# Optimization experiments

Measured on AMD Instinct MI355X. Metric: run time of the kernel, lower is better.

## Reference

```python
import jax, jax.numpy as jnp
import numpy as np

B, T, CIN, H, W = 8, 16, 16, 64, 64
HID, K = 64, 3


def _conv(x, w, b):
    # x: [B, C, H, W], w: [O, C, K, K] -> [B, O, H, W], 'same' padding
    y = jax.lax.conv_general_dilated(x, w, window_strides=(1, 1), padding='SAME',
                                     dimension_numbers=('NCHW', 'OIHW', 'NCHW'))
    return y + b[None, :, None, None]


def setup_inputs() -> dict:
    key = jax.random.key(0)
    ks = jax.random.split(key, 9)
    cin_h = CIN + HID
    s_conv = 1.0 / np.sqrt(cin_h * K * K)
    s_lin = 1.0 / np.sqrt(cin_h)
    return {
        'x': jax.random.normal(ks[0], (B, T, CIN, H, W), dtype=jnp.float32),
        'Wf': jax.random.uniform(ks[1], (HID, cin_h, K, K), jnp.float32, -s_conv, s_conv),
        'bf': jax.random.uniform(ks[2], (HID,), jnp.float32, -s_conv, s_conv),
        'Wi': jax.random.uniform(ks[3], (HID, cin_h, K, K), jnp.float32, -s_conv, s_conv),
        'bi': jax.random.uniform(ks[4], (HID,), jnp.float32, -s_conv, s_conv),
        'Wc': jax.random.uniform(ks[5], (HID, cin_h, K, K), jnp.float32, -s_conv, s_conv),
        'bc': jax.random.uniform(ks[6], (HID,), jnp.float32, -s_conv, s_conv),
        'Wo': jax.random.uniform(ks[7], (HID, cin_h), jnp.float32, -s_lin, s_lin),
        'bo': jax.random.uniform(ks[8], (HID,), jnp.float32, -s_lin, s_lin),
    }


def reference(x, Wf, bf, Wi, bi, Wc, bc, Wo, bo):
    # x: [B, T, CIN, H, W]
    b, t, cin, h, w = x.shape
    h0 = jnp.zeros((b, HID, h, w), x.dtype)
    c0 = jnp.zeros((b, HID, h, w), x.dtype)

    def step(carry, xt):
        hs, cs = carry
        xc = jnp.concatenate([xt, hs], axis=1)          # [B, CIN+HID, H, W]
        f = jax.nn.sigmoid(_conv(xc, Wf, bf))
        i = jax.nn.sigmoid(_conv(xc, Wi, bi))
        g = jnp.tanh(_conv(xc, Wc, bc))
        # Linear over channel dim (torch applies it on transpose(1,3))
        o = jax.nn.sigmoid(jnp.einsum('bchw,oc->bohw', xc, Wo) + bo[None, :, None, None])
        cs = cs * f + i * g
        hs = jnp.tanh(cs) * o
        return (hs, cs), None

    xs = jnp.swapaxes(x, 0, 1)                          # time-major [T, B, CIN, H, W]
    (hT, cT), _ = jax.lax.scan(step, (h0, c0), xs)
    return hT, cT
```

## Files before the change

### kernel.cpp

```cpp
#include <hip/hip_runtime.h>


#define B_ 8
#define T_ 16
#define CIN_ 16
#define HID_ 64
#define H_ 64
#define W_ 64
#define HW_ (H_*W_)
#define CTOT_ 80
#define XS_ROW 34
#define XS_CH 104
#define XS_SIZE (3*XS_ROW*XS_CH)
#define CSTRIDE_ (B_*HID_*HW_)

typedef __attribute__((ext_vector_type(8))) short short8;
typedef __attribute__((ext_vector_type(4))) float f32x4;

__device__ __forceinline__ unsigned short f2bf(float f){
    unsigned u = __float_as_uint(f);
    u = (u + 0x7FFFu + ((u >> 16) & 1u)) >> 16;
    return (unsigned short)u;
}
__device__ __forceinline__ float sigm_(float v){ return 1.0f/(1.0f + __expf(-v)); }
__device__ __forceinline__ float tanh_(float v){ return 2.0f/(1.0f + __expf(-2.0f*v)) - 1.0f; }

__global__ void prep_wfrag(const float* __restrict__ Wf, const float* __restrict__ Wi,
                           const float* __restrict__ Wc, const float* __restrict__ Wo,
                           const float* __restrict__ bf, const float* __restrict__ bi,
                           const float* __restrict__ bc, const float* __restrict__ bo,
                           unsigned short* __restrict__ Wfrag){
    int idx = blockIdx.x*256 + threadIdx.x;
    int j    = idx & 7;
    int lane = (idx >> 3) & 63;
    int frag = idx >> 9;
    int ng = frag & 15;
    int tc = frag >> 4;
    int cc = tc % 3, tap = tc / 3;
    int n = ng*16 + (lane & 15);
    int g = n >> 6, o = n & 63;
    int c = cc*32 + ((lane >> 4) << 3) + j;
    int ky = tap / 3, kx = tap % 3;
    float v = 0.0f;
    if (c < CTOT_){
        if (g == 0)      v = Wf[((o*CTOT_ + c)*3 + ky)*3 + kx];
        else if (g == 1) v = Wi[((o*CTOT_ + c)*3 + ky)*3 + kx];
        else if (g == 2) v = Wc[((o*CTOT_ + c)*3 + ky)*3 + kx];
        else             v = (tap == 4) ? Wo[o*CTOT_ + c] : 0.0f;
    } else if (c == CTOT_ && tap == 4){
        v = (g==0) ? bf[o] : (g==1) ? bi[o] : (g==2) ? bc[o] : bo[o];
    }
    Wfrag[idx] = f2bf(v);
}

__global__ void prep_xbf(const float* __restrict__ x, unsigned short* __restrict__ xbf){
    int idx = blockIdx.x*256 + threadIdx.x;
    int px = idx & 63;
    int y  = (idx >> 6) & 63;
    int bt = idx >> 12;
    const float* src = x + (size_t)bt*CIN_*HW_ + y*W_ + px;
    unsigned short tmp[16];
    #pragma unroll
    for (int c = 0; c < 16; ++c) tmp[c] = f2bf(src[(size_t)c*HW_]);
    uint4* dst = (uint4*)(xbf + (size_t)idx*16);
    dst[0] = *(uint4*)(tmp);
    dst[1] = *(uint4*)(tmp + 8);
}

__global__ __launch_bounds__(256, 4) void lstm_step(
    const unsigned short* __restrict__ xbf,
    const unsigned short* __restrict__ Wfrag,
    float* __restrict__ cbuf,
    const unsigned short* __restrict__ hin,
    unsigned short* __restrict__ hout,
    float* __restrict__ out,
    int t)
{
    __shared__ __align__(16) unsigned short Xs[XS_SIZE];
    const int id   = blockIdx.x;
    const int xcd  = id & 7;
    const int jj   = id >> 3;
    const int y    = xcd*8 + (jj & 7);
    const int b    = (jj >> 3) & 7;
    const int half = jj >> 6;
    const int x0   = half*32;
    const int tid  = threadIdx.x;
    const int lane = tid & 63;
    const int w    = tid >> 6;
    const int l15  = lane & 15;
    const int q    = lane >> 4;

    uint4 z4; z4.x=z4.y=z4.z=z4.w=0u;
    for (int i = tid; i < XS_SIZE/8; i += 256) ((uint4*)Xs)[i] = z4;
    __syncthreads();

    for (int i = tid; i < 204; i += 256){
        int row = i/68, rem = i - row*68;
        int px = rem >> 1, ch8 = rem & 1;
        int yy = y + row - 1, pxg = x0 + px - 1;
        if (yy >= 0 && yy < H_ && pxg >= 0 && pxg < W_){
            uint4 v = *(const uint4*)(xbf + ((((size_t)(b*T_ + t)*H_ + yy)*W_ + pxg)*16 + ch8*8));
            *(uint4*)(Xs + (row*XS_ROW + px)*XS_CH + ch8*8) = v;
        }
    }
    if (t > 0){
        for (int i = tid; i < 816; i += 256){
            int row = i/272, rem = i - row*272;
            int px = rem >> 3, ch8 = rem & 7;
            int yy = y + row - 1, pxg = x0 + px - 1;
            if (yy >= 0 && yy < H_ && pxg >= 0 && pxg < W_){
                uint4 v = *(const uint4*)(hin + ((((size_t)b*H_ + yy)*W_ + pxg)*HID_ + ch8*8));
                *(uint4*)(Xs + (row*XS_ROW + px)*XS_CH + CIN_ + ch8*8) = v;
            }
        }
    }
    for (int i = tid; i < 3*XS_ROW; i += 256)
        Xs[i*XS_CH + CTOT_] = 0x3F80;
    __syncthreads();

    f32x4 acc[4][2];
    #pragma unroll
    for (int g = 0; g < 4; ++g){ acc[g][0] = (f32x4)0.0f; acc[g][1] = (f32x4)0.0f; }

    short8 aC[2], bC[3], bO;
    {
        const unsigned short* ap = Xs + (size_t)l15*XS_CH + q*8;
        aC[0] = *(const short8*)(ap);
        aC[1] = *(const short8*)(ap + 16*XS_CH);
        const unsigned short* bp = Wfrag + (size_t)w*512 + lane*8;
        #pragma unroll
        for (int g = 0; g < 3; ++g) bC[g] = *(const short8*)(bp + ((size_t)g << 11));
    }
    for (int cc = 0; cc < 3; ++cc){
        #pragma unroll 1
        for (int tap = 0; tap < 9; ++tap){
            int ncc = cc, ntap = tap + 1;
            if (ntap == 9){ ntap = 0; ++ncc; }
            const bool have = (ncc < 3);
            short8 aN[2], bN[3];
            if (have){
                const int nky = ntap/3, nkx = ntap - 3*(ntap/3);
                const unsigned short* ap =
                    Xs + (size_t)(nky*XS_ROW + l15 + nkx)*XS_CH + ncc*32 + q*8;
                aN[0] = *(const short8*)(ap);
                aN[1] = *(const short8*)(ap + 16*XS_CH);
                const unsigned short* bp =
                    Wfrag + ((size_t)((ntap*3 + ncc)*16 + w) << 9) + lane*8;
                #pragma unroll
                for (int g = 0; g < 3; ++g) bN[g] = *(const short8*)(bp + ((size_t)g << 11));
            }
            if (tap == 3)
                bO = *(const short8*)(Wfrag + ((size_t)((4*3 + cc)*16 + 12 + w) << 9) + lane*8);
            if (tap == 4){
                acc[3][0] = __builtin_amdgcn_mfma_f32_16x16x32_bf16(aC[0], bO, acc[3][0], 0,0,0);
                acc[3][1] = __builtin_amdgcn_mfma_f32_16x16x32_bf16(aC[1], bO, acc[3][1], 0,0,0);
            }
            #pragma unroll
            for (int g = 0; g < 3; ++g){
                acc[g][0] = __builtin_amdgcn_mfma_f32_16x16x32_bf16(aC[0], bC[g], acc[g][0], 0,0,0);
                acc[g][1] = __builtin_amdgcn_mfma_f32_16x16x32_bf16(aC[1], bC[g], acc[g][1], 0,0,0);
            }
            if (have){
                aC[0]=aN[0]; aC[1]=aN[1];
                bC[0]=bN[0]; bC[1]=bN[1]; bC[2]=bN[2];
            }
        }
    }

    const int o = w*16 + l15;
    #pragma unroll
    for (int mf = 0; mf < 2; ++mf){
        #pragma unroll
        for (int r = 0; r < 4; ++r){
            const int m = mf*16 + q*4 + r;
            const int pxg = x0 + m;
            const float fv = sigm_(acc[0][mf][r]);
            const float iv = sigm_(acc[1][mf][r]);
            const float gv = tanh_(acc[2][mf][r]);
            const float ov = sigm_(acc[3][mf][r]);
            const size_t cidx = (((size_t)(b*H_ + y)*W_ + pxg)*HID_ + o);
            const float cprev = t ? cbuf[cidx] : 0.0f;
            const float cn = cprev*fv + iv*gv;
            const float hn = tanh_(cn)*ov;
            if (t < T_-1){
                cbuf[cidx] = cn;
                hout[cidx] = f2bf(hn);
            } else {
                const size_t oidx = ((((size_t)(b*HID_ + o))*H_ + y)*W_ + pxg);
                out[oidx] = hn;
                out[CSTRIDE_ + oidx] = cn;
            }
        }
    }
}

extern "C" void kernel_launch(void* const* d_in, const int* in_sizes, int n_in,
                              void* d_out, int out_size, void* d_ws, size_t ws_size,
                              hipStream_t stream){
    const float* x  = (const float*)d_in[0];
    const float* Wf = (const float*)d_in[1];
    const float* bf = (const float*)d_in[2];
    const float* Wi = (const float*)d_in[3];
    const float* bi = (const float*)d_in[4];
    const float* Wc = (const float*)d_in[5];
    const float* bc = (const float*)d_in[6];
    const float* Wo = (const float*)d_in[7];
    const float* bo = (const float*)d_in[8];

    unsigned short* Wfrag = (unsigned short*)d_ws;
    unsigned short* xbf   = (unsigned short*)((char*)d_ws + 442368);
    float*          cbuf  = (float*)((char*)d_ws + 442368 + 16777216);
    unsigned short* hbfA  = (unsigned short*)((char*)d_ws + 442368 + 16777216 + 8388608);
    unsigned short* hbfB  = hbfA + CSTRIDE_;

    prep_wfrag<<<dim3(864), dim3(256), 0, stream>>>(Wf, Wi, Wc, Wo, bf, bi, bc, bo, Wfrag);
    prep_xbf<<<dim3(2048), dim3(256), 0, stream>>>(x, xbf);

    for (int t = 0; t < T_; ++t){
        const unsigned short* hi = (t & 1) ? hbfA : hbfB;
        unsigned short*       ho = (t & 1) ? hbfB : hbfA;
        lstm_step<<<dim3(1024), dim3(256), 0, stream>>>(
            xbf, Wfrag, cbuf, hi, ho, (float*)d_out, t);
    }
}
```

Baseline: 428.7 us.

## Process full image rows per block with deeper weight prefetch pipeline

Each block now computes a full 64-pixel row instead of half a row, doubling M-fragments per wave to reuse each loaded weight fragment across four MFMA rows and reducing halo reloads. The K-loop is fully unrolled with a three-slot ring buffer prefetching weights two steps ahead. This halves the grid to 512 blocks and raises LDS and register use, lowering occupancy and possibly leaving CUs underfilled.

```diff
diff --git a/kernel.cpp b/kernel.cpp
--- a/kernel.cpp
+++ b/kernel.cpp
@@ -9,7 +9,7 @@
 #define W_ 64
 #define HW_ (H_*W_)
 #define CTOT_ 80
-#define XS_ROW 34
+#define XS_ROW 66
 #define XS_CH 104
 #define XS_SIZE (3*XS_ROW*XS_CH)
 #define CSTRIDE_ (B_*HID_*HW_)
@@ -67,7 +67,7 @@
     dst[1] = *(uint4*)(tmp + 8);
 }
 
-__global__ __launch_bounds__(256, 4) void lstm_step(
+__global__ __launch_bounds__(256, 3) void lstm_step(
     const unsigned short* __restrict__ xbf,
     const unsigned short* __restrict__ Wfrag,
     float* __restrict__ cbuf,
@@ -82,8 +82,6 @@
     const int jj   = id >> 3;
     const int y    = xcd*8 + (jj & 7);
     const int b    = (jj >> 3) & 7;
-    const int half = jj >> 6;
-    const int x0   = half*32;
     const int tid  = threadIdx.x;
     const int lane = tid & 63;
     const int w    = tid >> 6;
@@ -94,20 +92,20 @@
     for (int i = tid; i < XS_SIZE/8; i += 256) ((uint4*)Xs)[i] = z4;
     __syncthreads();
 
-    for (int i = tid; i < 204; i += 256){
-        int row = i/68, rem = i - row*68;
+    for (int i = tid; i < 396; i += 256){
+        int row = i/132, rem = i - row*132;
         int px = rem >> 1, ch8 = rem & 1;
-        int yy = y + row - 1, pxg = x0 + px - 1;
+        int yy = y + row - 1, pxg = px - 1;
         if (yy >= 0 && yy < H_ && pxg >= 0 && pxg < W_){
             uint4 v = *(const uint4*)(xbf + ((((size_t)(b*T_ + t)*H_ + yy)*W_ + pxg)*16 + ch8*8));
             *(uint4*)(Xs + (row*XS_ROW + px)*XS_CH + ch8*8) = v;
         }
     }
     if (t > 0){
-        for (int i = tid; i < 816; i += 256){
-            int row = i/272, rem = i - row*272;
+        for (int i = tid; i < 1584; i += 256){
+            int row = i/528, rem = i - row*528;
             int px = rem >> 3, ch8 = rem & 7;
-            int yy = y + row - 1, pxg = x0 + px - 1;
+            int yy = y + row - 1, pxg = px - 1;
             if (yy >= 0 && yy < H_ && pxg >= 0 && pxg < W_){
                 uint4 v = *(const uint4*)(hin + ((((size_t)b*H_ + yy)*W_ + pxg)*HID_ + ch8*8));
                 *(uint4*)(Xs + (row*XS_ROW + px)*XS_CH + CIN_ + ch8*8) = v;
@@ -118,67 +116,71 @@
         Xs[i*XS_CH + CTOT_] = 0x3F80;
     __syncthreads();
 
-    f32x4 acc[4][2];
-    #pragma unroll
-    for (int g = 0; g < 4; ++g){ acc[g][0] = (f32x4)0.0f; acc[g][1] = (f32x4)0.0f; }
-
-    short8 aC[2], bC[3], bO;
+    f32x4 acc[4][4];
+    #pragma unroll
+    for (int g = 0; g < 4; ++g)
+        #pragma unroll
+        for (int mf = 0; mf < 4; ++mf) acc[g][mf] = (f32x4)0.0f;
+
+    short8 aC[4], bq[3][3], bqo[2];
     {
         const unsigned short* ap = Xs + (size_t)l15*XS_CH + q*8;
-        aC[0] = *(const short8*)(ap);
-        aC[1] = *(const short8*)(ap + 16*XS_CH);
-        const unsigned short* bp = Wfrag + (size_t)w*512 + lane*8;
-        #pragma unroll
-        for (int g = 0; g < 3; ++g) bC[g] = *(const short8*)(bp + ((size_t)g << 11));
-    }
-    for (int cc = 0; cc < 3; ++cc){
-        #pragma unroll 1
-        for (int tap = 0; tap < 9; ++tap){
-            int ncc = cc, ntap = tap + 1;
-            if (ntap == 9){ ntap = 0; ++ncc; }
-            const bool have = (ncc < 3);
-            short8 aN[2], bN[3];
-            if (have){
-                const int nky = ntap/3, nkx = ntap - 3*(ntap/3);
-                const unsigned short* ap =
-                    Xs + (size_t)(nky*XS_ROW + l15 + nkx)*XS_CH + ncc*32 + q*8;
-                aN[0] = *(const short8*)(ap);
-                aN[1] = *(const short8*)(ap + 16*XS_CH);
-                const unsigned short* bp =
-                    Wfrag + ((size_t)((ntap*3 + ncc)*16 + w) << 9) + lane*8;
-                #pragma unroll
-                for (int g = 0; g < 3; ++g) bN[g] = *(const short8*)(bp + ((size_t)g << 11));
-            }
-            if (tap == 3)
-                bO = *(const short8*)(Wfrag + ((size_t)((4*3 + cc)*16 + 12 + w) << 9) + lane*8);
-            if (tap == 4){
-                acc[3][0] = __builtin_amdgcn_mfma_f32_16x16x32_bf16(aC[0], bO, acc[3][0], 0,0,0);
-                acc[3][1] = __builtin_amdgcn_mfma_f32_16x16x32_bf16(aC[1], bO, acc[3][1], 0,0,0);
-            }
-            #pragma unroll
-            for (int g = 0; g < 3; ++g){
-                acc[g][0] = __builtin_amdgcn_mfma_f32_16x16x32_bf16(aC[0], bC[g], acc[g][0], 0,0,0);
-                acc[g][1] = __builtin_amdgcn_mfma_f32_16x16x32_bf16(aC[1], bC[g], acc[g][1], 0,0,0);
-            }
-            if (have){
-                aC[0]=aN[0]; aC[1]=aN[1];
-                bC[0]=bN[0]; bC[1]=bN[1]; bC[2]=bN[2];
-            }
+        #pragma unroll
+        for (int mf = 0; mf < 4; ++mf) aC[mf] = *(const short8*)(ap + (size_t)mf*16*XS_CH);
+        #pragma unroll
+        for (int kt = 0; kt < 2; ++kt){
+            const unsigned short* bp = Wfrag + ((size_t)(kt*3*16 + w) << 9) + lane*8;
+            #pragma unroll
+            for (int g = 0; g < 3; ++g) bq[kt][g] = *(const short8*)(bp + ((size_t)g << 11));
+        }
+    }
+    #pragma unroll
+    for (int kt = 0; kt < 27; ++kt){
+        const int tap = kt % 9, cc = kt / 9;
+        if (kt + 2 < 27){
+            const int pk = kt + 2, pt = pk % 9, pc = pk / 9;
+            const unsigned short* bp = Wfrag + ((size_t)((pt*3 + pc)*16 + w) << 9) + lane*8;
+            #pragma unroll
+            for (int g = 0; g < 3; ++g) bq[pk % 3][g] = *(const short8*)(bp + ((size_t)g << 11));
+            if (pt == 4)
+                bqo[pc & 1] = *(const short8*)(Wfrag + ((size_t)((4*3 + pc)*16 + 12 + w) << 9) + lane*8);
+        }
+        short8 aN[4];
+        if (kt + 1 < 27){
+            const int nk = kt + 1, nt = nk % 9, nc = nk / 9;
+            const int nky = nt / 3, nkx = nt % 3;
+            const unsigned short* ap =
+                Xs + (size_t)(nky*XS_ROW + l15 + nkx)*XS_CH + nc*32 + q*8;
+            #pragma unroll
+            for (int mf = 0; mf < 4; ++mf) aN[mf] = *(const short8*)(ap + (size_t)mf*16*XS_CH);
+        }
+        if (tap == 4){
+            #pragma unroll
+            for (int mf = 0; mf < 4; ++mf)
+                acc[3][mf] = __builtin_amdgcn_mfma_f32_16x16x32_bf16(aC[mf], bqo[cc & 1], acc[3][mf], 0,0,0);
+        }
+        #pragma unroll
+        for (int g = 0; g < 3; ++g)
+            #pragma unroll
+            for (int mf = 0; mf < 4; ++mf)
+                acc[g][mf] = __builtin_amdgcn_mfma_f32_16x16x32_bf16(aC[mf], bq[kt % 3][g], acc[g][mf], 0,0,0);
+        if (kt + 1 < 27){
+            #pragma unroll
+            for (int mf = 0; mf < 4; ++mf) aC[mf] = aN[mf];
         }
     }
 
     const int o = w*16 + l15;
     #pragma unroll
-    for (int mf = 0; mf < 2; ++mf){
+    for (int mf = 0; mf < 4; ++mf){
         #pragma unroll
         for (int r = 0; r < 4; ++r){
             const int m = mf*16 + q*4 + r;
-            const int pxg = x0 + m;
             const float fv = sigm_(acc[0][mf][r]);
             const float iv = sigm_(acc[1][mf][r]);
             const float gv = tanh_(acc[2][mf][r]);
             const float ov = sigm_(acc[3][mf][r]);
-            const size_t cidx = (((size_t)(b*H_ + y)*W_ + pxg)*HID_ + o);
+            const size_t cidx = (((size_t)(b*H_ + y)*W_ + m)*HID_ + o);
             const float cprev = t ? cbuf[cidx] : 0.0f;
             const float cn = cprev*fv + iv*gv;
             const float hn = tanh_(cn)*ov;
@@ -186,7 +188,7 @@
                 cbuf[cidx] = cn;
                 hout[cidx] = f2bf(hn);
             } else {
-                const size_t oidx = ((((size_t)(b*HID_ + o))*H_ + y)*W_ + pxg);
+                const size_t oidx = ((((size_t)(b*HID_ + o))*H_ + y)*W_ + m);
                 out[oidx] = hn;
                 out[CSTRIDE_ + oidx] = cn;
             }
@@ -219,7 +221,7 @@
     for (int t = 0; t < T_; ++t){
         const unsigned short* hi = (t & 1) ? hbfA : hbfB;
         unsigned short*       ho = (t & 1) ? hbfB : hbfA;
-        lstm_step<<<dim3(1024), dim3(256), 0, stream>>>(
+        lstm_step<<<dim3(512), dim3(256), 0, stream>>>(
             xbf, Wfrag, cbuf, hi, ho, (float*)d_out, t);
     }
 }
```

After: 474.8 us. 1.11x slower.

## Split K reduction across two wave groups per block with LDS partial-sum merge

Applied to the files above, without the earlier changes.

Doubles the block to 512 threads and splits the 27 (channel-chunk, tap) reduction steps between two groups of four waves. The second group writes its partial accumulators to shared memory and the first group adds them before the gate epilogue. At t=0 only the 9 input-channel steps are computed because h is zero, which skips work the old loop did on zero data. This raises the number of waves in flight per block to hide latency, at the cost of an extra barrier, an LDS round trip and an uneven split (13 vs 14 steps).

```diff
diff --git a/kernel.cpp b/kernel.cpp
--- a/kernel.cpp
+++ b/kernel.cpp
@@ -12,6 +12,8 @@
 #define XS_ROW 34
 #define XS_CH 104
 #define XS_SIZE (3*XS_ROW*XS_CH)
+#define SM_BYTES 32768
+#define KSPLIT 13
 #define CSTRIDE_ (B_*HID_*HW_)
 
 typedef __attribute__((ext_vector_type(8))) short short8;
@@ -67,7 +69,7 @@
     dst[1] = *(uint4*)(tmp + 8);
 }
 
-__global__ __launch_bounds__(256, 4) void lstm_step(
+__global__ __launch_bounds__(512, 4) void lstm_step(
     const unsigned short* __restrict__ xbf,
     const unsigned short* __restrict__ Wfrag,
     float* __restrict__ cbuf,
@@ -76,25 +78,29 @@
     float* __restrict__ out,
     int t)
 {
-    __shared__ __align__(16) unsigned short Xs[XS_SIZE];
+    __shared__ __align__(16) char smem[SM_BYTES];
+    unsigned short* Xs = (unsigned short*)smem;
+    float*          P  = (float*)smem;
+
     const int id   = blockIdx.x;
     const int xcd  = id & 7;
     const int jj   = id >> 3;
     const int y    = xcd*8 + (jj & 7);
     const int b    = (jj >> 3) & 7;
-    const int half = jj >> 6;
-    const int x0   = half*32;
+    const int x0   = (jj >> 6) * 32;
     const int tid  = threadIdx.x;
     const int lane = tid & 63;
     const int w    = tid >> 6;
+    const int wl   = w & 3;
+    const int wh   = w >> 2;
     const int l15  = lane & 15;
     const int q    = lane >> 4;
 
     uint4 z4; z4.x=z4.y=z4.z=z4.w=0u;
-    for (int i = tid; i < XS_SIZE/8; i += 256) ((uint4*)Xs)[i] = z4;
-    __syncthreads();
-
-    for (int i = tid; i < 204; i += 256){
+    for (int i = tid; i < XS_SIZE/8; i += 512) ((uint4*)Xs)[i] = z4;
+    __syncthreads();
+
+    for (int i = tid; i < 204; i += 512){
         int row = i/68, rem = i - row*68;
         int px = rem >> 1, ch8 = rem & 1;
         int yy = y + row - 1, pxg = x0 + px - 1;
@@ -104,7 +110,7 @@
         }
     }
     if (t > 0){
-        for (int i = tid; i < 816; i += 256){
+        for (int i = tid; i < 816; i += 512){
             int row = i/272, rem = i - row*272;
             int px = rem >> 3, ch8 = rem & 7;
             int yy = y + row - 1, pxg = x0 + px - 1;
@@ -114,7 +120,7 @@
             }
         }
     }
-    for (int i = tid; i < 3*XS_ROW; i += 256)
+    for (int i = tid; i < 3*XS_ROW; i += 512)
         Xs[i*XS_CH + CTOT_] = 0x3F80;
     __syncthreads();
 
@@ -122,35 +128,45 @@
     #pragma unroll
     for (int g = 0; g < 4; ++g){ acc[g][0] = (f32x4)0.0f; acc[g][1] = (f32x4)0.0f; }
 
-    short8 aC[2], bC[3], bO;
-    {
-        const unsigned short* ap = Xs + (size_t)l15*XS_CH + q*8;
-        aC[0] = *(const short8*)(ap);
-        aC[1] = *(const short8*)(ap + 16*XS_CH);
-        const unsigned short* bp = Wfrag + (size_t)w*512 + lane*8;
-        #pragma unroll
-        for (int g = 0; g < 3; ++g) bC[g] = *(const short8*)(bp + ((size_t)g << 11));
-    }
-    for (int cc = 0; cc < 3; ++cc){
-        #pragma unroll 1
-        for (int tap = 0; tap < 9; ++tap){
-            int ncc = cc, ntap = tap + 1;
-            if (ntap == 9){ ntap = 0; ++ncc; }
-            const bool have = (ncc < 3);
-            short8 aN[2], bN[3];
+    const int ktot = t ? 27 : 9;
+    int kbeg = wh ? KSPLIT : 0;
+    int kend = wh ? ktot   : KSPLIT;
+    if (kend > ktot) kend = ktot;
+    if (kbeg > kend) kbeg = kend;
+
+    if (kbeg < kend){
+        short8 aC[2], bC[3], bO;
+        {
+            const int tap = kbeg % 9, cc = kbeg / 9;
+            const int ky = tap/3, kx = tap%3;
+            const unsigned short* ap = Xs + (size_t)(ky*XS_ROW + l15 + kx)*XS_CH + cc*32 + q*8;
+            aC[0] = *(const short8*)ap;
+            aC[1] = *(const short8*)(ap + 16*XS_CH);
+            const unsigned short* bp = Wfrag + ((size_t)((tap*3 + cc)*16 + wl) << 9) + lane*8;
+            #pragma unroll
+            for (int g = 0; g < 3; ++g) bC[g] = *(const short8*)(bp + ((size_t)(g*4) << 9));
+            if (tap == 4)
+                bO = *(const short8*)(Wfrag + ((size_t)((4*3 + cc)*16 + 12 + wl) << 9) + lane*8);
+        }
+        for (int kt = kbeg; kt < kend; ++kt){
+            const int tap = kt % 9;
+            const int nk = kt + 1;
+            const bool have = (nk < kend);
+            short8 aN[2], bN[3], bOn;
             if (have){
-                const int nky = ntap/3, nkx = ntap - 3*(ntap/3);
+                const int nt = nk % 9, nc = nk / 9;
+                const int nky = nt/3, nkx = nt%3;
                 const unsigned short* ap =
-                    Xs + (size_t)(nky*XS_ROW + l15 + nkx)*XS_CH + ncc*32 + q*8;
-                aN[0] = *(const short8*)(ap);
+                    Xs + (size_t)(nky*XS_ROW + l15 + nkx)*XS_CH + nc*32 + q*8;
+                aN[0] = *(const short8*)ap;
                 aN[1] = *(const short8*)(ap + 16*XS_CH);
                 const unsigned short* bp =
-                    Wfrag + ((size_t)((ntap*3 + ncc)*16 + w) << 9) + lane*8;
+                    Wfrag + ((size_t)((nt*3 + nc)*16 + wl) << 9) + lane*8;
                 #pragma unroll
-                for (int g = 0; g < 3; ++g) bN[g] = *(const short8*)(bp + ((size_t)g << 11));
-            }
-            if (tap == 3)
-                bO = *(const short8*)(Wfrag + ((size_t)((4*3 + cc)*16 + 12 + w) << 9) + lane*8);
+                for (int g = 0; g < 3; ++g) bN[g] = *(const short8*)(bp + ((size_t)(g*4) << 9));
+                if (nt == 4)
+                    bOn = *(const short8*)(Wfrag + ((size_t)((4*3 + nc)*16 + 12 + wl) << 9) + lane*8);
+            }
             if (tap == 4){
                 acc[3][0] = __builtin_amdgcn_mfma_f32_16x16x32_bf16(aC[0], bO, acc[3][0], 0,0,0);
                 acc[3][1] = __builtin_amdgcn_mfma_f32_16x16x32_bf16(aC[1], bO, acc[3][1], 0,0,0);
@@ -163,32 +179,50 @@
             if (have){
                 aC[0]=aN[0]; aC[1]=aN[1];
                 bC[0]=bN[0]; bC[1]=bN[1]; bC[2]=bN[2];
-            }
-        }
-    }
-
-    const int o = w*16 + l15;
-    #pragma unroll
-    for (int mf = 0; mf < 2; ++mf){
+                if (nk % 9 == 4) bO = bOn;
+            }
+        }
+    }
+
+    __syncthreads();
+    if (wh == 1){
         #pragma unroll
-        for (int r = 0; r < 4; ++r){
-            const int m = mf*16 + q*4 + r;
-            const int pxg = x0 + m;
-            const float fv = sigm_(acc[0][mf][r]);
-            const float iv = sigm_(acc[1][mf][r]);
-            const float gv = tanh_(acc[2][mf][r]);
-            const float ov = sigm_(acc[3][mf][r]);
-            const size_t cidx = (((size_t)(b*H_ + y)*W_ + pxg)*HID_ + o);
-            const float cprev = t ? cbuf[cidx] : 0.0f;
-            const float cn = cprev*fv + iv*gv;
-            const float hn = tanh_(cn)*ov;
-            if (t < T_-1){
-                cbuf[cidx] = cn;
-                hout[cidx] = f2bf(hn);
-            } else {
-                const size_t oidx = ((((size_t)(b*HID_ + o))*H_ + y)*W_ + pxg);
-                out[oidx] = hn;
-                out[CSTRIDE_ + oidx] = cn;
+        for (int g = 0; g < 4; ++g)
+            #pragma unroll
+            for (int mf = 0; mf < 2; ++mf)
+                *(f32x4*)(P + (size_t)(((wl*4 + g)*2 + mf)*256 + lane*4)) = acc[g][mf];
+    }
+    __syncthreads();
+    if (wh == 0){
+        #pragma unroll
+        for (int g = 0; g < 4; ++g)
+            #pragma unroll
+            for (int mf = 0; mf < 2; ++mf)
+                acc[g][mf] += *(const f32x4*)(P + (size_t)(((wl*4 + g)*2 + mf)*256 + lane*4));
+
+        const int o = wl*16 + l15;
+        #pragma unroll
+        for (int mf = 0; mf < 2; ++mf){
+            #pragma unroll
+            for (int r = 0; r < 4; ++r){
+                const int m = mf*16 + q*4 + r;
+                const int pxg = x0 + m;
+                const float fv = sigm_(acc[0][mf][r]);
+                const float iv = sigm_(acc[1][mf][r]);
+                const float gv = tanh_(acc[2][mf][r]);
+                const float ov = sigm_(acc[3][mf][r]);
+                const size_t cidx = (((size_t)(b*H_ + y)*W_ + pxg)*HID_ + o);
+                const float cprev = t ? cbuf[cidx] : 0.0f;
+                const float cn = cprev*fv + iv*gv;
+                const float hn = tanh_(cn)*ov;
+                if (t < T_-1){
+                    cbuf[cidx] = cn;
+                    hout[cidx] = f2bf(hn);
+                } else {
+                    const size_t oidx = ((((size_t)(b*HID_ + o))*H_ + y)*W_ + pxg);
+                    out[oidx] = hn;
+                    out[CSTRIDE_ + oidx] = cn;
+                }
             }
         }
     }
@@ -219,7 +253,7 @@
     for (int t = 0; t < T_; ++t){
         const unsigned short* hi = (t & 1) ? hbfA : hbfB;
         unsigned short*       ho = (t & 1) ? hbfB : hbfA;
-        lstm_step<<<dim3(1024), dim3(256), 0, stream>>>(
+        lstm_step<<<dim3(1024), dim3(512), 0, stream>>>(
             xbf, Wfrag, cbuf, hi, ho, (float*)d_out, t);
     }
 }
```

After: 540.2 us. 1.26x slower.

## Read MFMA operands directly from padded global xh buffers instead of LDS staging

Applied to the files above, without the earlier changes.

Replaces per-block LDS staging of the input and hidden tiles with a pre-padded, zero-bordered global buffer holding x and h in one channel-contiguous layout. MFMA A-fragments are loaded straight from global memory, which removes both __syncthreads and the LDS zero-fill. Each step also converts and writes the next timestep's x slice into the ping-pong buffer, and skips the hidden-channel chunks at t=0. The cost is that 3x3 halo reuse now depends on the L1/L2 caches rather than LDS, so each block issues more global loads.

```diff
diff --git a/kernel.cpp b/kernel.cpp
--- a/kernel.cpp
+++ b/kernel.cpp
@@ -9,9 +9,11 @@
 #define W_ 64
 #define HW_ (H_*W_)
 #define CTOT_ 80
-#define XS_ROW 34
-#define XS_CH 104
-#define XS_SIZE (3*XS_ROW*XS_CH)
+#define XH_R 66
+#define XH_C 96
+#define XH_ROWS (XH_R*XH_C)
+#define XH_BAT (XH_R*XH_ROWS)
+#define XH_ELEMS (B_*XH_BAT)
 #define CSTRIDE_ (B_*HID_*HW_)
 
 typedef __attribute__((ext_vector_type(8))) short short8;
@@ -53,121 +55,108 @@
     Wfrag[idx] = f2bf(v);
 }
 
-__global__ void prep_xbf(const float* __restrict__ x, unsigned short* __restrict__ xbf){
+__global__ void prep_zero(unsigned short* __restrict__ xhA){
+    const int n8 = 2*XH_ELEMS/8;
+    uint4 z; z.x=z.y=z.z=z.w=0u;
+    for (int i = blockIdx.x*256 + threadIdx.x; i < n8; i += 262144)
+        ((uint4*)xhA)[i] = z;
+}
+
+__global__ void prep_fill(const float* __restrict__ x,
+                          unsigned short* __restrict__ xhA,
+                          unsigned short* __restrict__ xhB){
     int idx = blockIdx.x*256 + threadIdx.x;
-    int px = idx & 63;
-    int y  = (idx >> 6) & 63;
-    int bt = idx >> 12;
-    const float* src = x + (size_t)bt*CIN_*HW_ + y*W_ + px;
+    int px = idx & 63, y = (idx >> 6) & 63, b = idx >> 12;
+    const float* src = x + ((size_t)b*T_*CIN_)*HW_ + y*W_ + px;
     unsigned short tmp[16];
     #pragma unroll
     for (int c = 0; c < 16; ++c) tmp[c] = f2bf(src[(size_t)c*HW_]);
-    uint4* dst = (uint4*)(xbf + (size_t)idx*16);
-    dst[0] = *(uint4*)(tmp);
-    dst[1] = *(uint4*)(tmp + 8);
+    unsigned short* dst = xhA + (size_t)b*XH_BAT + (y+1)*XH_ROWS + (px+1)*XH_C;
+    *(uint4*)dst       = *(uint4*)tmp;
+    *(uint4*)(dst + 8) = *(uint4*)(tmp + 8);
+    for (int j = idx; j < 2*B_*XH_R*XH_R; j += 32768){
+        unsigned short* base = (j < B_*XH_R*XH_R) ? xhA : xhB;
+        int r = (j < B_*XH_R*XH_R) ? j : j - B_*XH_R*XH_R;
+        base[(size_t)r*XH_C + CTOT_] = 0x3F80;
+    }
 }
 
 __global__ __launch_bounds__(256, 4) void lstm_step(
-    const unsigned short* __restrict__ xbf,
+    const float* __restrict__ x,
     const unsigned short* __restrict__ Wfrag,
+    const unsigned short* __restrict__ xh_cur,
+    unsigned short* __restrict__ xh_next,
     float* __restrict__ cbuf,
-    const unsigned short* __restrict__ hin,
-    unsigned short* __restrict__ hout,
     float* __restrict__ out,
     int t)
 {
-    __shared__ __align__(16) unsigned short Xs[XS_SIZE];
     const int id   = blockIdx.x;
     const int xcd  = id & 7;
     const int jj   = id >> 3;
     const int y    = xcd*8 + (jj & 7);
     const int b    = (jj >> 3) & 7;
-    const int half = jj >> 6;
-    const int x0   = half*32;
+    const int x0   = (jj >> 6) * 32;
     const int tid  = threadIdx.x;
     const int lane = tid & 63;
     const int w    = tid >> 6;
     const int l15  = lane & 15;
     const int q    = lane >> 4;
 
-    uint4 z4; z4.x=z4.y=z4.z=z4.w=0u;
-    for (int i = tid; i < XS_SIZE/8; i += 256) ((uint4*)Xs)[i] = z4;
-    __syncthreads();
-
-    for (int i = tid; i < 204; i += 256){
-        int row = i/68, rem = i - row*68;
-        int px = rem >> 1, ch8 = rem & 1;
-        int yy = y + row - 1, pxg = x0 + px - 1;
-        if (yy >= 0 && yy < H_ && pxg >= 0 && pxg < W_){
-            uint4 v = *(const uint4*)(xbf + ((((size_t)(b*T_ + t)*H_ + yy)*W_ + pxg)*16 + ch8*8));
-            *(uint4*)(Xs + (row*XS_ROW + px)*XS_CH + ch8*8) = v;
-        }
-    }
-    if (t > 0){
-        for (int i = tid; i < 816; i += 256){
-            int row = i/272, rem = i - row*272;
-            int px = rem >> 3, ch8 = rem & 7;
-            int yy = y + row - 1, pxg = x0 + px - 1;
-            if (yy >= 0 && yy < H_ && pxg >= 0 && pxg < W_){
-                uint4 v = *(const uint4*)(hin + ((((size_t)b*H_ + yy)*W_ + pxg)*HID_ + ch8*8));
-                *(uint4*)(Xs + (row*XS_ROW + px)*XS_CH + CIN_ + ch8*8) = v;
-            }
-        }
-    }
-    for (int i = tid; i < 3*XS_ROW; i += 256)
-        Xs[i*XS_CH + CTOT_] = 0x3F80;
-    __syncthreads();
+    const unsigned short* xb = xh_cur + (size_t)b*XH_BAT;
 
     f32x4 acc[4][2];
     #pragma unroll
     for (int g = 0; g < 4; ++g){ acc[g][0] = (f32x4)0.0f; acc[g][1] = (f32x4)0.0f; }
 
+    const int ktot = t ? 27 : 9;
+
     short8 aC[2], bC[3], bO;
     {
-        const unsigned short* ap = Xs + (size_t)l15*XS_CH + q*8;
-        aC[0] = *(const short8*)(ap);
-        aC[1] = *(const short8*)(ap + 16*XS_CH);
-        const unsigned short* bp = Wfrag + (size_t)w*512 + lane*8;
-        #pragma unroll
-        for (int g = 0; g < 3; ++g) bC[g] = *(const short8*)(bp + ((size_t)g << 11));
-    }
-    for (int cc = 0; cc < 3; ++cc){
-        #pragma unroll 1
-        for (int tap = 0; tap < 9; ++tap){
-            int ncc = cc, ntap = tap + 1;
-            if (ntap == 9){ ntap = 0; ++ncc; }
-            const bool have = (ncc < 3);
-            short8 aN[2], bN[3];
-            if (have){
-                const int nky = ntap/3, nkx = ntap - 3*(ntap/3);
-                const unsigned short* ap =
-                    Xs + (size_t)(nky*XS_ROW + l15 + nkx)*XS_CH + ncc*32 + q*8;
-                aN[0] = *(const short8*)(ap);
-                aN[1] = *(const short8*)(ap + 16*XS_CH);
-                const unsigned short* bp =
-                    Wfrag + ((size_t)((ntap*3 + ncc)*16 + w) << 9) + lane*8;
-                #pragma unroll
-                for (int g = 0; g < 3; ++g) bN[g] = *(const short8*)(bp + ((size_t)g << 11));
-            }
-            if (tap == 3)
-                bO = *(const short8*)(Wfrag + ((size_t)((4*3 + cc)*16 + 12 + w) << 9) + lane*8);
-            if (tap == 4){
-                acc[3][0] = __builtin_amdgcn_mfma_f32_16x16x32_bf16(aC[0], bO, acc[3][0], 0,0,0);
-                acc[3][1] = __builtin_amdgcn_mfma_f32_16x16x32_bf16(aC[1], bO, acc[3][1], 0,0,0);
-            }
+        const unsigned short* ap = xb + (size_t)(y*XH_ROWS) + (x0 + l15)*XH_C + q*8;
+        aC[0] = *(const short8*)ap;
+        aC[1] = *(const short8*)(ap + 16*XH_C);
+        const unsigned short* bp = Wfrag + ((size_t)w << 9) + lane*8;
+        #pragma unroll
+        for (int g = 0; g < 3; ++g) bC[g] = *(const short8*)(bp + ((size_t)(g*4) << 9));
+    }
+    #pragma unroll 1
+    for (int kt = 0; kt < ktot; ++kt){
+        const int tap = kt % 9;
+        const int nk = kt + 1;
+        const bool have = (nk < ktot);
+        short8 aN[2], bN[3], bOn;
+        if (have){
+            const int nt = nk % 9, ncc = nk / 9;
+            const int nky = nt/3, nkx = nt - 3*(nt/3);
+            const unsigned short* ap =
+                xb + (size_t)((y + nky)*XH_ROWS) + (x0 + l15 + nkx)*XH_C + ncc*32 + q*8;
+            aN[0] = *(const short8*)ap;
+            aN[1] = *(const short8*)(ap + 16*XH_C);
+            const unsigned short* bp =
+                Wfrag + ((size_t)((nt*3 + ncc)*16 + w) << 9) + lane*8;
             #pragma unroll
-            for (int g = 0; g < 3; ++g){
-                acc[g][0] = __builtin_amdgcn_mfma_f32_16x16x32_bf16(aC[0], bC[g], acc[g][0], 0,0,0);
-                acc[g][1] = __builtin_amdgcn_mfma_f32_16x16x32_bf16(aC[1], bC[g], acc[g][1], 0,0,0);
-            }
-            if (have){
-                aC[0]=aN[0]; aC[1]=aN[1];
-                bC[0]=bN[0]; bC[1]=bN[1]; bC[2]=bN[2];
-            }
+            for (int g = 0; g < 3; ++g) bN[g] = *(const short8*)(bp + ((size_t)(g*4) << 9));
+            if (nt == 4)
+                bOn = *(const short8*)(Wfrag + ((size_t)((4*3 + nk/9)*16 + 12 + w) << 9) + lane*8);
+        }
+        if (tap == 4){
+            acc[3][0] = __builtin_amdgcn_mfma_f32_16x16x32_bf16(aC[0], bO, acc[3][0], 0,0,0);
+            acc[3][1] = __builtin_amdgcn_mfma_f32_16x16x32_bf16(aC[1], bO, acc[3][1], 0,0,0);
+        }
+        #pragma unroll
+        for (int g = 0; g < 3; ++g){
+            acc[g][0] = __builtin_amdgcn_mfma_f32_16x16x32_bf16(aC[0], bC[g], acc[g][0], 0,0,0);
+            acc[g][1] = __builtin_amdgcn_mfma_f32_16x16x32_bf16(aC[1], bC[g], acc[g][1], 0,0,0);
+        }
+        if (have){
+            aC[0]=aN[0]; aC[1]=aN[1];
+            bC[0]=bN[0]; bC[1]=bN[1]; bC[2]=bN[2];
+            if (nk % 9 == 4) bO = bOn;
         }
     }
 
     const int o = w*16 + l15;
+    unsigned short* xnb = xh_next + (size_t)b*XH_BAT;
     #pragma unroll
     for (int mf = 0; mf < 2; ++mf){
         #pragma unroll
@@ -184,12 +173,22 @@
             const float hn = tanh_(cn)*ov;
             if (t < T_-1){
                 cbuf[cidx] = cn;
-                hout[cidx] = f2bf(hn);
+                xnb[(size_t)(y+1)*XH_ROWS + (pxg+1)*XH_C + CIN_ + o] = f2bf(hn);
             } else {
                 const size_t oidx = ((((size_t)(b*HID_ + o))*H_ + y)*W_ + pxg);
                 out[oidx] = hn;
                 out[CSTRIDE_ + oidx] = cn;
             }
+        }
+    }
+
+    if (t < T_-1){
+        #pragma unroll
+        for (int it = 0; it < 2; ++it){
+            const int item = tid + it*256;
+            const int c = item >> 5, px = item & 31;
+            const float v = x[((size_t)(b*T_ + t + 1)*CIN_ + c)*HW_ + y*W_ + x0 + px];
+            xnb[(size_t)(y+1)*XH_ROWS + (x0 + px + 1)*XH_C + c] = f2bf(v);
         }
     }
 }
@@ -208,18 +207,18 @@
     const float* bo = (const float*)d_in[8];
 
     unsigned short* Wfrag = (unsigned short*)d_ws;
-    unsigned short* xbf   = (unsigned short*)((char*)d_ws + 442368);
-    float*          cbuf  = (float*)((char*)d_ws + 442368 + 16777216);
-    unsigned short* hbfA  = (unsigned short*)((char*)d_ws + 442368 + 16777216 + 8388608);
-    unsigned short* hbfB  = hbfA + CSTRIDE_;
+    float*          cbuf  = (float*)((char*)d_ws + 442368);
+    unsigned short* xhA   = (unsigned short*)((char*)d_ws + 442368 + 8388608);
+    unsigned short* xhB   = xhA + XH_ELEMS;
 
     prep_wfrag<<<dim3(864), dim3(256), 0, stream>>>(Wf, Wi, Wc, Wo, bf, bi, bc, bo, Wfrag);
-    prep_xbf<<<dim3(2048), dim3(256), 0, stream>>>(x, xbf);
+    prep_zero<<<dim3(1024), dim3(256), 0, stream>>>(xhA);
+    prep_fill<<<dim3(128), dim3(256), 0, stream>>>(x, xhA, xhB);
 
     for (int t = 0; t < T_; ++t){
-        const unsigned short* hi = (t & 1) ? hbfA : hbfB;
-        unsigned short*       ho = (t & 1) ? hbfB : hbfA;
+        const unsigned short* xc = (t & 1) ? xhB : xhA;
+        unsigned short*       xn = (t & 1) ? xhA : xhB;
         lstm_step<<<dim3(1024), dim3(256), 0, stream>>>(
-            xbf, Wfrag, cbuf, hi, ho, (float*)d_out, t);
-    }
-}
+            x, Wfrag, xc, xn, cbuf, (float*)d_out, t);
+    }
+}
```

After: 592.6 us. 1.38x slower.
